# Kernel tuning notes

Measured on AMD Instinct MI355X. Metric: run time of the kernel, lower is better.

Reference implementation:

```python
import jax, jax.numpy as jnp
import numpy as np

B, S, D, H = 2, 2048, 1024, 16
HD = D // H

def setup_inputs() -> dict:
    key = jax.random.key(0)
    ks = jax.random.split(key, 5)
    s = 1.0 / np.sqrt(D)
    return {
        "x": jax.random.normal(ks[0], (B, S, D), dtype=jnp.float32),
        "Wq": jax.random.normal(ks[1], (D, D), dtype=jnp.float32) * s,
        "Wk": jax.random.normal(ks[2], (D, D), dtype=jnp.float32) * s,
        "Wv": jax.random.normal(ks[3], (D, D), dtype=jnp.float32) * s,
        "Wo": jax.random.normal(ks[4], (D, D), dtype=jnp.float32) * s,
        "bo": jnp.zeros((D,), dtype=jnp.float32),
    }

def reference(x, Wq, Wk, Wv, Wo, bo):
    b, n, _ = x.shape
    # QKV projections (no bias), reshape to [B, H, S, HD]
    def proj(W):
        return (x @ W.T).reshape(b, n, H, HD).transpose(0, 2, 1, 3)
    q, k, v = proj(Wq), proj(Wk), proj(Wv)
    scores = jnp.einsum("bhqd,bhkd->bhqk", q, k)
    causal = jnp.triu(jnp.ones((n, n), dtype=bool), k=1)
    scores = jnp.where(causal, -jnp.inf, scores)
    attn = jax.nn.softmax(scores / np.sqrt(HD), axis=-1)  # dropout p=0.0 (eval)
    ctx = jnp.einsum("bhqk,bhkd->bhqd", attn, v)
    ctx = ctx.transpose(0, 2, 1, 3).reshape(b, n, D)
    return ctx @ Wo.T + bo
```

## Files before the change

### kernel.cpp

```cpp
#include <hip/hip_runtime.h>
#include <stdint.h>


typedef __bf16 bf16_t;
typedef __bf16 bf16x8 __attribute__((ext_vector_type(8)));
typedef float  f32x4  __attribute__((ext_vector_type(4)));
typedef uint32_t u32x4 __attribute__((ext_vector_type(4)));

#define MFMA16(A, B, C) __builtin_amdgcn_mfma_f32_16x16x32_bf16(A, B, C, 0, 0, 0)

__device__ __forceinline__ void async_ld16(const bf16_t* g, bf16_t* l) {
  __builtin_amdgcn_global_load_lds(
      (const __attribute__((address_space(1))) void*)g,
      (__attribute__((address_space(3))) void*)l, 16, 0, 0);
}

__device__ __forceinline__ u32x4 ld8(const float* p) {
  const float4 a = *(const float4*)p;
  const float4 b = *(const float4*)(p + 4);
  union { u32x4 v; bf16_t h[8]; } r;
  r.h[0] = (bf16_t)a.x; r.h[1] = (bf16_t)a.y;
  r.h[2] = (bf16_t)a.z; r.h[3] = (bf16_t)a.w;
  r.h[4] = (bf16_t)b.x; r.h[5] = (bf16_t)b.y;
  r.h[6] = (bf16_t)b.z; r.h[7] = (bf16_t)b.w;
  return r.v;
}

__global__ __launch_bounds__(256) void cvt_all(
    const float* __restrict__ sx, const float* __restrict__ s1,
    const float* __restrict__ s2, const float* __restrict__ s3,
    bf16_t* __restrict__ dx, bf16_t* __restrict__ d1,
    bf16_t* __restrict__ d2, bf16_t* __restrict__ d3) {
  const int y = blockIdx.y;
  if (y != 0 && blockIdx.x >= 1024) return;
  const int i4 = (blockIdx.x * 256 + threadIdx.x) * 4;
  const float* s = (y == 0) ? sx : (y == 1) ? s1 : (y == 2) ? s2 : s3;
  bf16_t*      d = (y == 0) ? dx : (y == 1) ? d1 : (y == 2) ? d2 : d3;
  const float4 v = *(const float4*)(s + i4);
  union { uint64_t u; bf16_t h[4]; } pk;
  pk.h[0] = (bf16_t)v.x; pk.h[1] = (bf16_t)v.y;
  pk.h[2] = (bf16_t)v.z; pk.h[3] = (bf16_t)v.w;
  *(uint64_t*)(d + i4) = pk.u;
}

__global__ __launch_bounds__(256, 2) void gemm_qkv_a(
    const bf16_t* __restrict__ X,  const bf16_t* __restrict__ Wq,
    const bf16_t* __restrict__ Wk, const bf16_t* __restrict__ Wv,
    bf16_t* __restrict__ Q, bf16_t* __restrict__ K, bf16_t* __restrict__ V) {
  const int z = blockIdx.z;
  const bf16_t* W = (z == 0) ? Wq : (z == 1) ? Wk : Wv;
  bf16_t*       D = (z == 0) ? Q  : (z == 1) ? K  : V;
  const int mode = (z == 2) ? 1 : 0;

  __shared__ __align__(16) bf16_t As[128 * 64];
  __shared__ __align__(16) bf16_t Bs[128 * 64];

  const int tid  = threadIdx.x;
  const int lane = tid & 63;
  const int w    = tid >> 6;
  const int quad = lane >> 4;
  const int l15  = lane & 15;
  const int bm   = blockIdx.y * 128;
  const int bn   = blockIdx.x * 128;
  const int wm   = (w >> 1) * 64;
  const int wn   = (w & 1) * 64;
  const int sr   = lane >> 3;
  const int sc   = lane & 7;

  f32x4 acc[4][4] = {};

  for (int k0 = 0; k0 < 1024; k0 += 64) {
#pragma unroll
    for (int j = 0; j < 4; ++j) {
      const int r0 = w * 32 + j * 8;
      const int r  = r0 + sr;
      const int c  = sc ^ (r & 7);
      async_ld16(X + (size_t)(bm + r) * 1024 + k0 + c * 8, &As[r0 * 64]);
      async_ld16(W + (size_t)(bn + r) * 1024 + k0 + c * 8, &Bs[r0 * 64]);
    }
    __syncthreads();
#pragma unroll
    for (int kk = 0; kk < 64; kk += 32) {
      const int ck = (kk >> 3) + quad;
      bf16x8 aF[4], bF[4];
#pragma unroll
      for (int mt = 0; mt < 4; ++mt) {
        const int r = wm + mt * 16 + l15;
        aF[mt] = *(const bf16x8*)&As[r * 64 + (ck ^ (r & 7)) * 8];
      }
#pragma unroll
      for (int nt = 0; nt < 4; ++nt) {
        const int r = wn + nt * 16 + l15;
        bF[nt] = *(const bf16x8*)&Bs[r * 64 + (ck ^ (r & 7)) * 8];
      }
#pragma unroll
      for (int mt = 0; mt < 4; ++mt)
#pragma unroll
        for (int nt = 0; nt < 4; ++nt)
          acc[mt][nt] = MFMA16(aF[mt], bF[nt], acc[mt][nt]);
    }
    __syncthreads();
  }

#pragma unroll
  for (int mt = 0; mt < 4; ++mt) {
#pragma unroll
    for (int nt = 0; nt < 4; ++nt) {
      const int n  = bn + wn + nt * 16 + l15;
      const int mb = bm + wm + mt * 16 + quad * 4;
      const int h = n >> 6, hd = n & 63;
      if (mode == 0) {
#pragma unroll
        for (int r = 0; r < 4; ++r) {
          const int m = mb + r;
          const int b = m >> 11, s = m & 2047;
          D[(size_t)b * 2097152 + (size_t)h * 131072 + (size_t)s * 64 + hd] =
              (bf16_t)acc[mt][nt][r];
        }
      } else {
        const int b = mb >> 11, s0 = mb & 2047;
        union { uint64_t u; bf16_t h4[4]; } pk;
#pragma unroll
        for (int r = 0; r < 4; ++r) pk.h4[r] = (bf16_t)acc[mt][nt][r];
        *(uint64_t*)(D + (size_t)b * 2097152 + (size_t)h * 131072 +
                     (size_t)hd * 2048 + s0) = pk.u;
      }
    }
  }
}

__global__ __launch_bounds__(256, 2) void gemm_out_m(
    const bf16_t* __restrict__ ctx, const float* __restrict__ Wo,
    float* __restrict__ out, const float* __restrict__ bo) {
  __shared__ __align__(16) bf16_t As[64 * 64];
  __shared__ __align__(16) bf16_t Bs[128 * 64];

  const int tid  = threadIdx.x;
  const int lane = tid & 63;
  const int w    = tid >> 6;
  const int quad = lane >> 4;
  const int l15  = lane & 15;
  const int bm   = blockIdx.y * 64;
  const int bn   = blockIdx.x * 128;
  const int wm   = (w >> 1) * 32;
  const int wn   = (w & 1) * 64;
  const int sr   = lane >> 3;
  const int sc   = lane & 7;
  const int srow = tid >> 3;
  const int schk = tid & 7;

  f32x4 acc[2][4] = {};

  for (int k0 = 0; k0 < 1024; k0 += 64) {
#pragma unroll
    for (int j = 0; j < 2; ++j) {
      const int r0 = w * 16 + j * 8;
      const int r  = r0 + sr;
      const int c  = sc ^ (r & 7);
      async_ld16(ctx + (size_t)(bm + r) * 1024 + k0 + c * 8, &As[r0 * 64]);
    }
    u32x4 rb[4];
#pragma unroll
    for (int s2 = 0; s2 < 4; ++s2) {
      const int r = srow + s2 * 32;
      rb[s2] = ld8(Wo + (size_t)(bn + r) * 1024 + k0 + schk * 8);
    }
#pragma unroll
    for (int s2 = 0; s2 < 4; ++s2) {
      const int r = srow + s2 * 32;
      *(u32x4*)&Bs[r * 64 + ((schk ^ (r & 7)) * 8)] = rb[s2];
    }
    __syncthreads();
#pragma unroll
    for (int kk = 0; kk < 64; kk += 32) {
      const int ck = (kk >> 3) + quad;
      bf16x8 aF[2], bF[4];
#pragma unroll
      for (int mt = 0; mt < 2; ++mt) {
        const int r = wm + mt * 16 + l15;
        aF[mt] = *(const bf16x8*)&As[r * 64 + (ck ^ (r & 7)) * 8];
      }
#pragma unroll
      for (int nt = 0; nt < 4; ++nt) {
        const int r = wn + nt * 16 + l15;
        bF[nt] = *(const bf16x8*)&Bs[r * 64 + (ck ^ (r & 7)) * 8];
      }
#pragma unroll
      for (int mt = 0; mt < 2; ++mt)
#pragma unroll
        for (int nt = 0; nt < 4; ++nt)
          acc[mt][nt] = MFMA16(aF[mt], bF[nt], acc[mt][nt]);
    }
    __syncthreads();
  }

#pragma unroll
  for (int mt = 0; mt < 2; ++mt) {
#pragma unroll
    for (int nt = 0; nt < 4; ++nt) {
      const int n  = bn + wn + nt * 16 + l15;
      const int mb = bm + wm + mt * 16 + quad * 4;
      const float bv = bo[n];
#pragma unroll
      for (int r = 0; r < 4; ++r)
        out[(size_t)(mb + r) * 1024 + n] = acc[mt][nt][r] + bv;
    }
  }
}

__global__ __launch_bounds__(256, 4) void attn(
    const bf16_t* __restrict__ Qw, const bf16_t* __restrict__ Kw,
    const bf16_t* __restrict__ Vw, bf16_t* __restrict__ ctx) {
  constexpr int LDK = 72, LDV = 72, LDP = 72;
  __shared__ __align__(16) bf16_t Ks[64 * LDK];
  __shared__ __align__(16) bf16_t Vts[64 * LDV];
  __shared__ __align__(16) bf16_t Ps[64 * LDP];

  const int tid  = threadIdx.x;
  const int lane = tid & 63;
  const int w    = tid >> 6;
  const int quad = lane >> 4;
  const int l15  = lane & 15;
  const int h    = blockIdx.y;
  const int b    = blockIdx.z;
  const int x    = blockIdx.x;
  const int u    = (b << 1) | ((h >> 3) & 1);
  const int r64  = (u == 0) ? x
                 : (u == 1) ? (31 - x)
                 : (u == 2) ? ((x + 16) & 31)
                            : ((15 - x) & 31);
  const size_t bh = (size_t)(b * 16 + h) * (size_t)(2048 * 64);
  const bf16_t* Qh = Qw + bh;
  const bf16_t* Kh = Kw + bh;
  const bf16_t* Vh = Vw + bh;

  const int srl = lane >> 3, scl = lane & 7;

  {
    const int srow = tid >> 3, sch = tid & 7;
    u32x4 rq[2];
#pragma unroll
    for (int s2 = 0; s2 < 2; ++s2)
      rq[s2] = *(const u32x4*)(Qh + (size_t)(r64 * 64 + srow + s2 * 32) * 64 + sch * 8);
#pragma unroll
    for (int s2 = 0; s2 < 2; ++s2)
      *(u32x4*)&Ps[(srow + s2 * 32) * LDP + sch * 8] = rq[s2];
  }
  __syncthreads();
  bf16x8 qF[2];
#pragma unroll
  for (int k2 = 0; k2 < 2; ++k2)
    qF[k2] = *(const bf16x8*)&Ps[(w * 16 + l15) * LDP + k2 * 32 + quad * 8];

  f32x4 O[4] = {};
  float mrow = -1e30f, lrow = 0.f;
  const float sc_log2 = 0.125f * 1.44269504088896340736f;
  const float DTHR = 44.0f;

  u32x4 rk[2], rv[2];
#pragma unroll
  for (int j = 0; j < 2; ++j)
    rk[j] = *(const u32x4*)(Kh + (size_t)(w * 16 + j * 8 + srl) * 64 + scl * 8);
#pragma unroll
  for (int j = 0; j < 2; ++j)
    rv[j] = *(const u32x4*)(Vh + (size_t)(w * 16 + j * 8 + srl) * 2048 + scl * 8);

  for (int kt = 0; kt <= r64; ++kt) {
    __syncthreads();
#pragma unroll
    for (int j = 0; j < 2; ++j)
      *(u32x4*)&Ks[(w * 16 + j * 8 + srl) * LDK + scl * 8] = rk[j];
#pragma unroll
    for (int j = 0; j < 2; ++j)
      *(u32x4*)&Vts[(w * 16 + j * 8 + srl) * LDV + scl * 8] = rv[j];
    __syncthreads();

    if (kt < r64) {
      const int kn = kt + 1;
#pragma unroll
      for (int j = 0; j < 2; ++j)
        rk[j] = *(const u32x4*)(Kh + (size_t)(kn * 64 + w * 16 + j * 8 + srl) * 64 + scl * 8);
#pragma unroll
      for (int j = 0; j < 2; ++j)
        rv[j] = *(const u32x4*)(Vh + (size_t)(w * 16 + j * 8 + srl) * 2048 + kn * 64 + scl * 8);
    }

    f32x4 St[4] = {};
    __builtin_amdgcn_s_setprio(1);
#pragma unroll
    for (int ntk = 0; ntk < 4; ++ntk) {
      const int kr = ntk * 16 + l15;
#pragma unroll
      for (int k2 = 0; k2 < 2; ++k2) {
        const bf16x8 kF = *(const bf16x8*)&Ks[kr * LDK + k2 * 32 + quad * 8];
        St[ntk] = MFMA16(kF, qF[k2], St[ntk]);
      }
    }
    __builtin_amdgcn_s_setprio(0);

    if (kt == r64) {
      const int ql = w * 16 + l15;
#pragma unroll
      for (int ntk = 0; ntk < 4; ++ntk)
#pragma unroll
        for (int r = 0; r < 4; ++r)
          if (ntk * 16 + quad * 4 + r > ql) St[ntk][r] = -1e30f;
    }

    float mx = -1e30f;
#pragma unroll
    for (int ntk = 0; ntk < 4; ++ntk)
#pragma unroll
      for (int r = 0; r < 4; ++r) mx = fmaxf(mx, St[ntk][r]);
    mx = fmaxf(mx, __shfl_xor(mx, 16));
    mx = fmaxf(mx, __shfl_xor(mx, 32));

    float alpha = 1.f;
    if (!__all(mx - mrow <= DTHR)) {
      const float mnew = fmaxf(mrow, mx);
      alpha = exp2f((mrow - mnew) * sc_log2);
      mrow = mnew;
#pragma unroll
      for (int r = 0; r < 4; ++r) {
        const float a = __shfl(alpha, quad * 4 + r);
#pragma unroll
        for (int nt = 0; nt < 4; ++nt) O[nt][r] *= a;
      }
    }

    float rs = 0.f;
#pragma unroll
    for (int ntk = 0; ntk < 4; ++ntk) {
      union { uint64_t u64; bf16_t h4[4]; } pk;
#pragma unroll
      for (int r = 0; r < 4; ++r) {
        const float p = exp2f((St[ntk][r] - mrow) * sc_log2);
        rs += p;
        pk.h4[r] = (bf16_t)p;
      }
      *(uint64_t*)&Ps[(w * 16 + l15) * LDP + ntk * 16 + quad * 4] = pk.u64;
    }
    rs += __shfl_xor(rs, 16);
    rs += __shfl_xor(rs, 32);
    lrow = lrow * alpha + rs;

    __builtin_amdgcn_s_setprio(1);
#pragma unroll
    for (int kk = 0; kk < 64; kk += 32) {
      const int co = kk + quad * 8;
      const bf16x8 pF = *(const bf16x8*)&Ps[(w * 16 + l15) * LDP + co];
      bf16x8 vF[4];
#pragma unroll
      for (int nt = 0; nt < 4; ++nt)
        vF[nt] = *(const bf16x8*)&Vts[(nt * 16 + l15) * LDV + co];
#pragma unroll
      for (int nt = 0; nt < 4; ++nt)
        O[nt] = MFMA16(pF, vF[nt], O[nt]);
    }
    __builtin_amdgcn_s_setprio(0);
  }

#pragma unroll
  for (int r = 0; r < 4; ++r) {
    const float lr = __shfl(lrow, quad * 4 + r);
    const float iv = 1.f / lr;
    const int s = r64 * 64 + w * 16 + quad * 4 + r;
#pragma unroll
    for (int nt = 0; nt < 4; ++nt) {
      const int hd = nt * 16 + l15;
      ctx[(size_t)(b * 2048 + s) * 1024 + h * 64 + hd] =
          (bf16_t)(O[nt][r] * iv);
    }
  }
}

extern "C" void kernel_launch(void* const* d_in, const int* in_sizes, int n_in,
                              void* d_out, int out_size, void* d_ws, size_t ws_size,
                              hipStream_t stream) {
  const float* x  = (const float*)d_in[0];
  const float* Wq = (const float*)d_in[1];
  const float* Wk = (const float*)d_in[2];
  const float* Wv = (const float*)d_in[3];
  const float* Wo = (const float*)d_in[4];
  const float* bo = (const float*)d_in[5];

  bf16_t* ws   = (bf16_t*)d_ws;
  bf16_t* Qw   = ws;
  bf16_t* Kw   = ws + 4194304;
  bf16_t* Vw   = ws + 8388608;
  bf16_t* ctxw = ws + 12582912;

  bf16_t* dscr = (bf16_t*)d_out;
  bf16_t* xb   = dscr;
  bf16_t* Wqb  = dscr + 4194304;
  bf16_t* Wkb  = dscr + 5242880;
  bf16_t* Wvb  = dscr + 6291456;
  float*  out  = (float*)d_out;

  dim3 blk(256);
  cvt_all<<<dim3(4096, 4), blk, 0, stream>>>(x, Wq, Wk, Wv, xb, Wqb, Wkb, Wvb);
  gemm_qkv_a<<<dim3(8, 32, 3), blk, 0, stream>>>(xb, Wqb, Wkb, Wvb, Qw, Kw, Vw);
  attn<<<dim3(32, 16, 2), blk, 0, stream>>>(Qw, Kw, Vw, ctxw);
  gemm_out_m<<<dim3(8, 64), blk, 0, stream>>>(ctxw, Wo, out, bo);
}
```

Baseline: 187.3 us.

## Pre-convert Wo to bf16 and stream it into LDS asynchronously

Adds a separate conversion kernel that turns Wo into bf16, writing it into the Q workspace buffer, which is dead once attention has finished. The output GEMM then loads its B tile with async global-to-LDS copies instead of fp32 register loads, in-kernel conversion and LDS stores. This removes per-tile conversion and register staging from the output GEMM's inner loop, at the cost of an extra kernel launch and a 4 MB fp32 read plus 2 MB bf16 write. The QKV GEMM's launch bounds are also raised to target 3 blocks per SIMD.

Measured after the change: 181.4 us, median of 2. 3.2% less time.

```diff
diff --git a/kernel.cpp b/kernel.cpp
--- a/kernel.cpp
+++ b/kernel.cpp
@@ -13,17 +13,6 @@
   __builtin_amdgcn_global_load_lds(
       (const __attribute__((address_space(1))) void*)g,
       (__attribute__((address_space(3))) void*)l, 16, 0, 0);
-}
-
-__device__ __forceinline__ u32x4 ld8(const float* p) {
-  const float4 a = *(const float4*)p;
-  const float4 b = *(const float4*)(p + 4);
-  union { u32x4 v; bf16_t h[8]; } r;
-  r.h[0] = (bf16_t)a.x; r.h[1] = (bf16_t)a.y;
-  r.h[2] = (bf16_t)a.z; r.h[3] = (bf16_t)a.w;
-  r.h[4] = (bf16_t)b.x; r.h[5] = (bf16_t)b.y;
-  r.h[6] = (bf16_t)b.z; r.h[7] = (bf16_t)b.w;
-  return r.v;
 }
 
 __global__ __launch_bounds__(256) void cvt_all(
@@ -43,7 +32,17 @@
   *(uint64_t*)(d + i4) = pk.u;
 }
 
-__global__ __launch_bounds__(256, 2) void gemm_qkv_a(
+__global__ __launch_bounds__(256) void cvt_wo(
+    const float* __restrict__ s, bf16_t* __restrict__ d) {
+  const int i4 = (blockIdx.x * 256 + threadIdx.x) * 4;
+  const float4 v = *(const float4*)(s + i4);
+  union { uint64_t u; bf16_t h[4]; } pk;
+  pk.h[0] = (bf16_t)v.x; pk.h[1] = (bf16_t)v.y;
+  pk.h[2] = (bf16_t)v.z; pk.h[3] = (bf16_t)v.w;
+  *(uint64_t*)(d + i4) = pk.u;
+}
+
+__global__ __launch_bounds__(256, 3) void gemm_qkv_a(
     const bf16_t* __restrict__ X,  const bf16_t* __restrict__ Wq,
     const bf16_t* __restrict__ Wk, const bf16_t* __restrict__ Wv,
     bf16_t* __restrict__ Q, bf16_t* __restrict__ K, bf16_t* __restrict__ V) {
@@ -129,8 +128,8 @@
   }
 }
 
-__global__ __launch_bounds__(256, 2) void gemm_out_m(
-    const bf16_t* __restrict__ ctx, const float* __restrict__ Wo,
+__global__ __launch_bounds__(256, 2) void gemm_out_a(
+    const bf16_t* __restrict__ ctx, const bf16_t* __restrict__ Wob,
     float* __restrict__ out, const float* __restrict__ bo) {
   __shared__ __align__(16) bf16_t As[64 * 64];
   __shared__ __align__(16) bf16_t Bs[128 * 64];
@@ -146,8 +145,6 @@
   const int wn   = (w & 1) * 64;
   const int sr   = lane >> 3;
   const int sc   = lane & 7;
-  const int srow = tid >> 3;
-  const int schk = tid & 7;
 
   f32x4 acc[2][4] = {};
 
@@ -159,16 +156,12 @@
       const int c  = sc ^ (r & 7);
       async_ld16(ctx + (size_t)(bm + r) * 1024 + k0 + c * 8, &As[r0 * 64]);
     }
-    u32x4 rb[4];
-#pragma unroll
-    for (int s2 = 0; s2 < 4; ++s2) {
-      const int r = srow + s2 * 32;
-      rb[s2] = ld8(Wo + (size_t)(bn + r) * 1024 + k0 + schk * 8);
-    }
-#pragma unroll
-    for (int s2 = 0; s2 < 4; ++s2) {
-      const int r = srow + s2 * 32;
-      *(u32x4*)&Bs[r * 64 + ((schk ^ (r & 7)) * 8)] = rb[s2];
+#pragma unroll
+    for (int j = 0; j < 4; ++j) {
+      const int r0 = w * 32 + j * 8;
+      const int r  = r0 + sr;
+      const int c  = sc ^ (r & 7);
+      async_ld16(Wob + (size_t)(bn + r) * 1024 + k0 + c * 8, &Bs[r0 * 64]);
     }
     __syncthreads();
 #pragma unroll
@@ -389,6 +382,7 @@
   bf16_t* Kw   = ws + 4194304;
   bf16_t* Vw   = ws + 8388608;
   bf16_t* ctxw = ws + 12582912;
+  bf16_t* Wob  = Qw;
 
   bf16_t* dscr = (bf16_t*)d_out;
   bf16_t* xb   = dscr;
@@ -401,5 +395,6 @@
   cvt_all<<<dim3(4096, 4), blk, 0, stream>>>(x, Wq, Wk, Wv, xb, Wqb, Wkb, Wvb);
   gemm_qkv_a<<<dim3(8, 32, 3), blk, 0, stream>>>(xb, Wqb, Wkb, Wvb, Qw, Kw, Vw);
   attn<<<dim3(32, 16, 2), blk, 0, stream>>>(Qw, Kw, Vw, ctxw);
-  gemm_out_m<<<dim3(8, 64), blk, 0, stream>>>(ctxw, Wo, out, bo);
-}
+  cvt_wo<<<dim3(1024), blk, 0, stream>>>(Wo, Wob);
+  gemm_out_a<<<dim3(8, 64), blk, 0, stream>>>(ctxw, Wob, out, bo);
+}
```
